# Kernel tuning notes

Hardware: AMD Instinct MI355X
Metric: run time of the kernel (lower is better)

## Reference

```python
import jax, jax.numpy as jnp
import numpy as np

ITER_ROUTING = 50
EPS = 1e-9


def _squash(z):
    # z: [..., D]; TF code uses reduce_mean of squares over the feature axis
    ns = jnp.mean(jnp.square(z), axis=-1, keepdims=True)
    return ns * z / ((1.0 + ns) * jnp.sqrt(ns + EPS))


def setup_inputs() -> dict:
    key = jax.random.key(0)
    k1, k2, k3 = jax.random.split(key, 3)
    B, S, Din = 2048, 200, 64  # batch, behavior_size, behavior_ndim
    K, D = 8, 64               # interest_size, interest_ndim
    inputs = jax.random.normal(k1, (B, S, Din), dtype=jnp.float32)
    W = jax.random.normal(k2, (Din, D), dtype=jnp.float32) * (1.0 / np.sqrt(Din))
    bias = jnp.zeros((D,), dtype=jnp.float32)
    b_init = jax.random.normal(k3, (B, S, K), dtype=jnp.float32)
    return {"inputs": inputs, "W": W, "bias": bias, "b_init": b_init}


def reference(inputs, W, bias, b_init):
    # v_ij = Dense(inputs): identical every iteration in the original -> compute once
    v = inputs @ W + bias  # [B, S, D]

    def routing_step(b, _):
        w = jax.nn.softmax(b, axis=1)                  # softmax over behaviors, per interest
        z = jnp.einsum('bsk,bsd->bkd', w, v)           # weighted sum over behaviors
        u = _squash(z)                                 # [B, K, D]
        b = b + jnp.einsum('bsd,bkd->bsk', v, u)       # agreement update
        return b, None

    # iter_routing-1 update steps, then one final readout (u_js are taken from the
    # last iteration BEFORE its b update, so compute it separately).
    b, _ = jax.lax.scan(routing_step, b_init, None, length=ITER_ROUTING - 1)
    w = jax.nn.softmax(b, axis=1)
    u = _squash(jnp.einsum('bsk,bsd->bkd', w, v))      # [B, K, D]
    return u
```

## Files before the change

kernel.cpp:

```cpp
#include <hip/hip_runtime.h>

#define NITERS 50

typedef __attribute__((ext_vector_type(4))) float f32x4;
typedef __attribute__((ext_vector_type(8))) _Float16 f16x8;
typedef __attribute__((ext_vector_type(4))) _Float16 f16x4;

#define STL_OFF 9216
#define SE_F 1632
#define SQP_F 1640
#define EF_H 3400
#define ZN_H 7208

#define L2E 1.44269504f

struct HL {
  _Float16 h, l;
};
__device__ __forceinline__ HL split2(float x) {
  HL r;
  r.h = (_Float16)x;
  r.l = (_Float16)(x - (float)r.h);
  return r;
}

template <int CTRL>
__device__ __forceinline__ float dppmv(float x) {
  return __int_as_float(__builtin_amdgcn_update_dpp(
      0, __float_as_int(x), CTRL, 0xF, 0xF, true));
}
__device__ __forceinline__ float swz16(float x) {
  return __int_as_float(
      __builtin_amdgcn_ds_swizzle(__float_as_int(x), 0x401F));
}
__device__ __forceinline__ float wave_red_add(float x) {
  x += dppmv<0x121>(x);
  x += dppmv<0x122>(x);
  x += dppmv<0x124>(x);
  x += dppmv<0x128>(x);
  x += swz16(x);
  x += __shfl_xor(x, 32, 64);
  return x;
}
__device__ __forceinline__ float wave_red_max(float x) {
  x = fmaxf(x, dppmv<0x121>(x));
  x = fmaxf(x, dppmv<0x122>(x));
  x = fmaxf(x, dppmv<0x124>(x));
  x = fmaxf(x, dppmv<0x128>(x));
  x = fmaxf(x, swz16(x));
  x = fmaxf(x, __shfl_xor(x, 32, 64));
  return x;
}

__global__ __launch_bounds__(256, 3) void mie7(
    const float* __restrict__ gin, const float* __restrict__ gW,
    const float* __restrict__ gbias, const float* __restrict__ gb0,
    float* __restrict__ gout) {
  __shared__ short arena[18432];
  float* smF = (float*)arena;
  _Float16* smH = (_Float16*)arena;
  _Float16* sth = smH;
  _Float16* stl = smH + STL_OFF;

  const int b = blockIdx.x;
  const int tid = threadIdx.x;
  const int wv = tid >> 6;
  const int lane = tid & 63;
  const int col = lane & 15;
  const int oct = lane >> 4;
  const int kcol = col & 7;
  const int d0 = wv * 16;

  f16x8 wh[2], wl[2];
#pragma unroll
  for (int c = 0; c < 2; ++c)
#pragma unroll
    for (int j = 0; j < 8; ++j) {
      HL t = split2(gW[(32 * c + oct * 8 + j) * 64 + d0 + col]);
      wh[c][j] = t.h;
      wl[c][j] = t.l;
    }
  float biasc = gbias[d0 + col];
  const float* ginb = gin + (size_t)b * 12800;

  f16x8 vBh[7], vBl[7];
  f16x8 vCh[4][2], vCl[4][2];

  auto compute_rows = [&](int mtA, int mtB, int rb) {
#pragma unroll 2
    for (int mt = mtA; mt < mtB; ++mt) {
      int sa = mt * 16 + col;
      f16x8 ah[2] = {{}, {}}, al[2] = {{}, {}};
      if (sa < 200) {
#pragma unroll
        for (int c = 0; c < 2; ++c) {
          const float* p = ginb + sa * 64 + 32 * c + oct * 8;
          float4 x0 = *(const float4*)p;
          float4 x1 = *(const float4*)(p + 4);
          HL t0 = split2(x0.x), t1 = split2(x0.y), t2 = split2(x0.z),
             t3 = split2(x0.w);
          HL t4 = split2(x1.x), t5 = split2(x1.y), t6 = split2(x1.z),
             t7 = split2(x1.w);
          ah[c][0] = t0.h; al[c][0] = t0.l;
          ah[c][1] = t1.h; al[c][1] = t1.l;
          ah[c][2] = t2.h; al[c][2] = t2.l;
          ah[c][3] = t3.h; al[c][3] = t3.l;
          ah[c][4] = t4.h; al[c][4] = t4.l;
          ah[c][5] = t5.h; al[c][5] = t5.l;
          ah[c][6] = t6.h; al[c][6] = t6.l;
          ah[c][7] = t7.h; al[c][7] = t7.l;
        }
      }
      f32x4 acc = {0.f, 0.f, 0.f, 0.f};
#pragma unroll
      for (int c = 0; c < 2; ++c) {
        acc = __builtin_amdgcn_mfma_f32_16x16x32_f16(ah[c], wh[c], acc, 0, 0, 0);
        acc = __builtin_amdgcn_mfma_f32_16x16x32_f16(ah[c], wl[c], acc, 0, 0, 0);
        acc = __builtin_amdgcn_mfma_f32_16x16x32_f16(al[c], wh[c], acc, 0, 0, 0);
      }
#pragma unroll
      for (int r = 0; r < 4; ++r) {
        int so = mt * 16 + oct * 4 + r;
        if (so < 200) {
          HL t = split2(acc[r] + biasc);
          sth[(so - rb) * 72 + d0 + col] = t.h;
          stl[(so - rb) * 72 + d0 + col] = t.l;
        }
      }
    }
  };

  compute_rows(0, 8, 0);
  __syncthreads();
#pragma unroll
  for (int t = 0; t < 4; ++t) {
#pragma unroll
    for (int j = 0; j < 8; ++j) {
      int sR = 32 * t + oct * 8 + j;
      vBh[t][j] = sth[sR * 72 + d0 + col];
      vBl[t][j] = stl[sR * 72 + d0 + col];
    }
  }
#pragma unroll
  for (int u = 0; u < 2; ++u) {
    int sR = (wv + 4 * u) * 16 + col;
#pragma unroll
    for (int c = 0; c < 2; ++c) {
      vCh[u][c] = *(const f16x8*)&sth[sR * 72 + 32 * c + oct * 8];
      vCl[u][c] = *(const f16x8*)&stl[sR * 72 + 32 * c + oct * 8];
    }
  }
  __syncthreads();

  compute_rows(8, 13, 128);
  __syncthreads();
#pragma unroll
  for (int t = 4; t < 7; ++t) {
    if (t < 6 || oct == 0) {
#pragma unroll
      for (int j = 0; j < 8; ++j) {
        int sR = 32 * t + oct * 8 + j - 128;
        vBh[t][j] = sth[sR * 72 + d0 + col];
        vBl[t][j] = stl[sR * 72 + d0 + col];
      }
    } else {
      vBh[t] = f16x8{};
      vBl[t] = f16x8{};
    }
  }
#pragma unroll
  for (int u = 2; u < 4; ++u) {
    int mt = wv + 4 * u;
    if (mt < 13) {
      int sR = mt * 16 + col;
      if (sR > 199) sR = 199;
      sR -= 128;
#pragma unroll
      for (int c = 0; c < 2; ++c) {
        vCh[u][c] = *(const f16x8*)&sth[sR * 72 + 32 * c + oct * 8];
        vCl[u][c] = *(const f16x8*)&stl[sR * 72 + 32 * c + oct * 8];
      }
    } else {
#pragma unroll
      for (int c = 0; c < 2; ++c) {
        vCh[u][c] = f16x8{};
        vCl[u][c] = f16x8{};
      }
    }
  }
  __syncthreads();

  const float* gb = gb0 + (size_t)b * 1600;
  for (int idx = tid; idx < 1600; idx += 256)
    smF[(idx & 7) * 204 + (idx >> 3)] = gb[idx] * L2E;
  __syncthreads();

#pragma unroll 1
  for (int it = 0; it < NITERS; ++it) {
#pragma unroll
    for (int ki = 0; ki < 2; ++ki) {
      int kk = 2 * wv + ki;
      float4 bv;
      if (lane < 50)
        bv = *(const float4*)&smF[kk * 204 + 4 * lane];
      else
        bv = make_float4(-3e38f, -3e38f, -3e38f, -3e38f);
      float mxa =
          wave_red_max(fmaxf(fmaxf(bv.x, bv.y), fmaxf(bv.z, bv.w))) - 12.f;
      float e0 = exp2f(bv.x - mxa);
      float e1 = exp2f(bv.y - mxa);
      float e2 = exp2f(bv.z - mxa);
      float e3 = exp2f(bv.w - mxa);
      HL s0 = split2(e0), s1 = split2(e1), s2 = split2(e2), s3 = split2(e3);
      f16x4 hv, lv;
      hv[0] = s0.h; lv[0] = s0.l;
      hv[1] = s1.h; lv[1] = s1.l;
      hv[2] = s2.h; lv[2] = s2.l;
      hv[3] = s3.h; lv[3] = s3.l;
      if (lane < 56) {
        int slot = (lane >> 1) * 136 + kk * 8 + (lane & 1) * 4;
        *(f16x4*)&smH[EF_H + slot] = hv;
        *(f16x4*)&smH[EF_H + slot + 64] = lv;
      }
      float se = wave_red_add((e0 + e1) + (e2 + e3));
      if (lane == 0) smF[SE_F + kk] = se;
    }
    __syncthreads();

    f32x4 z0 = {0.f, 0.f, 0.f, 0.f}, z1 = {0.f, 0.f, 0.f, 0.f};
#pragma unroll
    for (int t = 0; t < 7; ++t) {
      f16x8 ep = *(const f16x8*)&smH[EF_H + (t * 4 + oct) * 136 + col * 8];
      if (t & 1) {
        z1 = __builtin_amdgcn_mfma_f32_16x16x32_f16(vBh[t], ep, z1, 0, 0, 0);
        z1 = __builtin_amdgcn_mfma_f32_16x16x32_f16(vBl[t], ep, z1, 0, 0, 0);
      } else {
        z0 = __builtin_amdgcn_mfma_f32_16x16x32_f16(vBh[t], ep, z0, 0, 0, 0);
        z0 = __builtin_amdgcn_mfma_f32_16x16x32_f16(vBl[t], ep, z0, 0, 0, 0);
      }
    }
    f32x4 z = z0 + z1;
#pragma unroll
    for (int r = 0; r < 4; ++r) z[r] += dppmv<0x128>(z[r]);
    float sq = z[0] * z[0] + z[1] * z[1] + z[2] * z[2] + z[3] * z[3];
    sq += swz16(sq);
    sq += __shfl_xor(sq, 32, 64);
    if (oct == 0 && col < 8) smF[SQP_F + wv * 8 + col] = sq;
    {
      f16x4 st;
#pragma unroll
      for (int r = 0; r < 4; ++r) {
        float val = z[r] * (1.f / 4096.f);
        _Float16 h = (_Float16)val;
        st[r] = (col < 8) ? h : (_Float16)(val - (float)h);
      }
      int octf = (2 * wv + (oct >> 1)) & 3;
      int slot = ((wv >> 1) * 4 + octf) * 136 + col * 8 + (oct & 1) * 4;
      *(f16x4*)&smH[ZN_H + slot] = st;
    }
    __syncthreads();

    float sqt = smF[SQP_F + kcol] + smF[SQP_F + 8 + kcol] +
                smF[SQP_F + 16 + kcol] + smF[SQP_F + 24 + kcol];
    float Se = smF[SE_F + kcol];
    float rse = __builtin_amdgcn_rcpf(Se);
    float ns = sqt * 0.015625f * rse * rse;
    float cv = ns * __builtin_amdgcn_rsqf(ns + 1e-9f) *
               __builtin_amdgcn_rcpf(1.f + ns) * rse;

    if (it == NITERS - 1) {
      if (col < 8) {
        float4 u4;
        u4.x = cv * z[0];
        u4.y = cv * z[1];
        u4.z = cv * z[2];
        u4.w = cv * z[3];
        *(float4*)&gout[(size_t)b * 512 + col * 64 + 16 * wv + 4 * oct] = u4;
      }
    } else {
      float cvC = cv * (4096.f * L2E);
      f16x8 zf0 = *(const f16x8*)&smH[ZN_H + oct * 136 + col * 8];
      f16x8 zf1 = *(const f16x8*)&smH[ZN_H + (4 + oct) * 136 + col * 8];
#pragma unroll
      for (int u = 0; u < 4; ++u) {
        int mt = wv + 4 * u;
        if (mt < 13) {
          f32x4 a = {0.f, 0.f, 0.f, 0.f};
          a = __builtin_amdgcn_mfma_f32_16x16x32_f16(vCh[u][0], zf0, a, 0, 0, 0);
          a = __builtin_amdgcn_mfma_f32_16x16x32_f16(vCl[u][0], zf0, a, 0, 0, 0);
          a = __builtin_amdgcn_mfma_f32_16x16x32_f16(vCh[u][1], zf1, a, 0, 0, 0);
          a = __builtin_amdgcn_mfma_f32_16x16x32_f16(vCl[u][1], zf1, a, 0, 0, 0);
#pragma unroll
          for (int r = 0; r < 4; ++r) a[r] += dppmv<0x128>(a[r]);
          if (col < 8) {
            int s0 = mt * 16 + 4 * oct;
            if (s0 < 200) {
              float* bp = &smF[col * 204 + s0];
              float4 bb = *(float4*)bp;
              bb.x = fmaf(cvC, a[0], bb.x);
              bb.y = fmaf(cvC, a[1], bb.y);
              bb.z = fmaf(cvC, a[2], bb.z);
              bb.w = fmaf(cvC, a[3], bb.w);
              *(float4*)bp = bb;
            }
          }
        }
      }
    }
    __syncthreads();
  }
}

extern "C" void kernel_launch(void* const* d_in, const int* in_sizes, int n_in,
                              void* d_out, int out_size, void* d_ws,
                              size_t ws_size, hipStream_t stream) {
  const float* gin = (const float*)d_in[0];
  const float* gW = (const float*)d_in[1];
  const float* gbias = (const float*)d_in[2];
  const float* gb0 = (const float*)d_in[3];
  float* gout = (float*)d_out;
  hipLaunchKernelGGL(mie7, dim3(2048), dim3(256), 0, stream, gin, gW, gbias,
                     gb0, gout);
}
```

Baseline: 355.5 us.

## Fuse softmax max into routing update and shorten sum reductions

Each wave now records the per-interest maximum of the routing logits while it applies the agreement update. Those partial maxima go to shared memory, so the next iteration's softmax reads four values instead of running a full cross-wave max reduction. The exp-sum reduction stops at 16-lane groups and the four partials are added later. The MFMA chains are also split into four independent accumulators to expose more instruction-level parallelism. This removes the dependent DPP/swizzle/shuffle reduction chains from each iteration, at the cost of a few extra shared-memory reads and writes.

After: 354.8 us. Within noise of the previous version (-0.2%).

```diff
diff --git a/kernel.cpp b/kernel.cpp
--- a/kernel.cpp
+++ b/kernel.cpp
@@ -7,10 +7,11 @@
 typedef __attribute__((ext_vector_type(4))) _Float16 f16x4;
 
 #define STL_OFF 9216
-#define SE_F 1632
 #define SQP_F 1640
 #define EF_H 3400
 #define ZN_H 7208
+#define SEP_F 4160
+#define MX_F 4200
 
 #define L2E 1.44269504f
 
@@ -33,15 +34,6 @@
   return __int_as_float(
       __builtin_amdgcn_ds_swizzle(__float_as_int(x), 0x401F));
 }
-__device__ __forceinline__ float wave_red_add(float x) {
-  x += dppmv<0x121>(x);
-  x += dppmv<0x122>(x);
-  x += dppmv<0x124>(x);
-  x += dppmv<0x128>(x);
-  x += swz16(x);
-  x += __shfl_xor(x, 32, 64);
-  return x;
-}
 __device__ __forceinline__ float wave_red_max(float x) {
   x = fmaxf(x, dppmv<0x121>(x));
   x = fmaxf(x, dppmv<0x122>(x));
@@ -52,7 +44,7 @@
   return x;
 }
 
-__global__ __launch_bounds__(256, 3) void mie7(
+__global__ __launch_bounds__(256, 3) void mie8(
     const float* __restrict__ gin, const float* __restrict__ gW,
     const float* __restrict__ gbias, const float* __restrict__ gb0,
     float* __restrict__ gout) {
@@ -195,18 +187,37 @@
     smF[(idx & 7) * 204 + (idx >> 3)] = gb[idx] * L2E;
   __syncthreads();
 
+#pragma unroll
+  for (int ki = 0; ki < 2; ++ki) {
+    int kk = 2 * wv + ki;
+    float4 bv;
+    if (lane < 50)
+      bv = *(const float4*)&smF[kk * 204 + 4 * lane];
+    else
+      bv = make_float4(-3e38f, -3e38f, -3e38f, -3e38f);
+    float mx = wave_red_max(fmaxf(fmaxf(bv.x, bv.y), fmaxf(bv.z, bv.w)));
+    if (lane == 0) {
+      smF[MX_F + kk] = mx;
+      smF[MX_F + 8 + kk] = mx;
+      smF[MX_F + 16 + kk] = mx;
+      smF[MX_F + 24 + kk] = mx;
+    }
+  }
+  __syncthreads();
+
 #pragma unroll 1
   for (int it = 0; it < NITERS; ++it) {
 #pragma unroll
     for (int ki = 0; ki < 2; ++ki) {
       int kk = 2 * wv + ki;
+      float mx01 = fmaxf(smF[MX_F + kk], smF[MX_F + 8 + kk]);
+      float mx23 = fmaxf(smF[MX_F + 16 + kk], smF[MX_F + 24 + kk]);
+      float mxa = fmaxf(mx01, mx23) - 12.f;
       float4 bv;
       if (lane < 50)
         bv = *(const float4*)&smF[kk * 204 + 4 * lane];
       else
         bv = make_float4(-3e38f, -3e38f, -3e38f, -3e38f);
-      float mxa =
-          wave_red_max(fmaxf(fmaxf(bv.x, bv.y), fmaxf(bv.z, bv.w))) - 12.f;
       float e0 = exp2f(bv.x - mxa);
       float e1 = exp2f(bv.y - mxa);
       float e2 = exp2f(bv.z - mxa);
@@ -222,24 +233,29 @@
         *(f16x4*)&smH[EF_H + slot] = hv;
         *(f16x4*)&smH[EF_H + slot + 64] = lv;
       }
-      float se = wave_red_add((e0 + e1) + (e2 + e3));
-      if (lane == 0) smF[SE_F + kk] = se;
+      float se = (e0 + e1) + (e2 + e3);
+      se += dppmv<0x121>(se);
+      se += dppmv<0x122>(se);
+      se += dppmv<0x124>(se);
+      se += dppmv<0x128>(se);
+      if ((lane & 15) == 0) smF[SEP_F + kk * 4 + oct] = se;
     }
     __syncthreads();
 
-    f32x4 z0 = {0.f, 0.f, 0.f, 0.f}, z1 = {0.f, 0.f, 0.f, 0.f};
+    f32x4 zc0 = {0.f, 0.f, 0.f, 0.f}, zc1 = {0.f, 0.f, 0.f, 0.f};
+    f32x4 zc2 = {0.f, 0.f, 0.f, 0.f}, zc3 = {0.f, 0.f, 0.f, 0.f};
 #pragma unroll
     for (int t = 0; t < 7; ++t) {
       f16x8 ep = *(const f16x8*)&smH[EF_H + (t * 4 + oct) * 136 + col * 8];
       if (t & 1) {
-        z1 = __builtin_amdgcn_mfma_f32_16x16x32_f16(vBh[t], ep, z1, 0, 0, 0);
-        z1 = __builtin_amdgcn_mfma_f32_16x16x32_f16(vBl[t], ep, z1, 0, 0, 0);
+        zc2 = __builtin_amdgcn_mfma_f32_16x16x32_f16(vBh[t], ep, zc2, 0, 0, 0);
+        zc3 = __builtin_amdgcn_mfma_f32_16x16x32_f16(vBl[t], ep, zc3, 0, 0, 0);
       } else {
-        z0 = __builtin_amdgcn_mfma_f32_16x16x32_f16(vBh[t], ep, z0, 0, 0, 0);
-        z0 = __builtin_amdgcn_mfma_f32_16x16x32_f16(vBl[t], ep, z0, 0, 0, 0);
-      }
-    }
-    f32x4 z = z0 + z1;
+        zc0 = __builtin_amdgcn_mfma_f32_16x16x32_f16(vBh[t], ep, zc0, 0, 0, 0);
+        zc1 = __builtin_amdgcn_mfma_f32_16x16x32_f16(vBl[t], ep, zc1, 0, 0, 0);
+      }
+    }
+    f32x4 z = (zc0 + zc1) + (zc2 + zc3);
 #pragma unroll
     for (int r = 0; r < 4; ++r) z[r] += dppmv<0x128>(z[r]);
     float sq = z[0] * z[0] + z[1] * z[1] + z[2] * z[2] + z[3] * z[3];
@@ -262,7 +278,8 @@
 
     float sqt = smF[SQP_F + kcol] + smF[SQP_F + 8 + kcol] +
                 smF[SQP_F + 16 + kcol] + smF[SQP_F + 24 + kcol];
-    float Se = smF[SE_F + kcol];
+    float Se = (smF[SEP_F + kcol * 4 + 0] + smF[SEP_F + kcol * 4 + 1]) +
+               (smF[SEP_F + kcol * 4 + 2] + smF[SEP_F + kcol * 4 + 3]);
     float rse = __builtin_amdgcn_rcpf(Se);
     float ns = sqt * 0.015625f * rse * rse;
     float cv = ns * __builtin_amdgcn_rsqf(ns + 1e-9f) *
@@ -281,6 +298,7 @@
       float cvC = cv * (4096.f * L2E);
       f16x8 zf0 = *(const f16x8*)&smH[ZN_H + oct * 136 + col * 8];
       f16x8 zf1 = *(const f16x8*)&smH[ZN_H + (4 + oct) * 136 + col * 8];
+      float bmax = -3e38f;
 #pragma unroll
       for (int u = 0; u < 4; ++u) {
         int mt = wv + 4 * u;
@@ -302,10 +320,15 @@
               bb.z = fmaf(cvC, a[2], bb.z);
               bb.w = fmaf(cvC, a[3], bb.w);
               *(float4*)bp = bb;
+              bmax = fmaxf(
+                  bmax, fmaxf(fmaxf(bb.x, bb.y), fmaxf(bb.z, bb.w)));
             }
           }
         }
       }
+      bmax = fmaxf(bmax, swz16(bmax));
+      bmax = fmaxf(bmax, __shfl_xor(bmax, 32, 64));
+      if (lane < 8) smF[MX_F + wv * 8 + lane] = bmax;
     }
     __syncthreads();
   }
@@ -319,6 +342,6 @@
   const float* gbias = (const float*)d_in[2];
   const float* gb0 = (const float*)d_in[3];
   float* gout = (float*)d_out;
-  hipLaunchKernelGGL(mie7, dim3(2048), dim3(256), 0, stream, gin, gW, gbias,
+  hipLaunchKernelGGL(mie8, dim3(2048), dim3(256), 0, stream, gin, gW, gbias,
                      gb0, gout);
 }
```
